# Optimization experiments

Measured on AMD Instinct MI355X. Metric: run time of the kernel, lower is better.

The kernel has to match this reference:

```python
import jax, jax.numpy as jnp
import numpy as np

B, T, H, O = 128, 512, 1024, 128


def setup_inputs() -> dict:
    key = jax.random.key(0)
    ks = jax.random.split(key, 9)
    s = 0.05  # small init scale for numerical sanity
    return {
        "y_hist": jax.random.normal(ks[0], (B, T), jnp.float32),
        "W_ih": jax.random.normal(ks[1], (4 * H, 1), jnp.float32) * s,
        "W_hh": jax.random.normal(ks[2], (4 * H, H), jnp.float32) * s,
        "b_ih": jax.random.normal(ks[3], (4 * H,), jnp.float32) * s,
        "b_hh": jax.random.normal(ks[4], (4 * H,), jnp.float32) * s,
        "fc_W": jax.random.normal(ks[5], (O, H), jnp.float32) * s,
        "fc_b": jax.random.normal(ks[6], (O,), jnp.float32) * s,
        # stands in for the xavier-initialized (1,B,H) h0/c0 of the original
        "h0": jax.random.normal(ks[7], (B, H), jnp.float32) * s,
        "c0": jax.random.normal(ks[8], (B, H), jnp.float32) * s,
    }


def reference(y_hist, W_ih, W_hh, b_ih, b_hh, fc_W, fc_b, h0, c0):
    # PyTorch LSTM cell, gate order (i, f, g, o); input feature size is 1.
    Hs = W_hh.shape[1]
    w_ih = W_ih[:, 0]          # (4H,)
    b = b_ih + b_hh            # (4H,)

    def step(carry, x_t):
        h, c = carry           # (B,H), (B,H)
        gates = h @ W_hh.T + x_t[:, None] * w_ih + b  # (B,4H)
        i, f, g, o = jnp.split(gates, 4, axis=-1)
        c = jax.nn.sigmoid(f) * c + jax.nn.sigmoid(i) * jnp.tanh(g)
        h = jax.nn.sigmoid(o) * jnp.tanh(c)
        return (h, c), None

    (h_T, _), _ = jax.lax.scan(step, (h0, c0), y_hist.T)  # scan over time (T,B)
    return h_T @ fc_W.T + fc_b  # (B, O)
```

## Files before the change

kernel.cpp:

```cpp
#include <hip/hip_runtime.h>
#include <hip/hip_fp16.h>

typedef _Float16 half8 __attribute__((ext_vector_type(8)));
typedef float f32x4 __attribute__((ext_vector_type(4)));

#define T_STEPS 512

__device__ __forceinline__ float sigf(float x) {
    return __builtin_amdgcn_rcpf(1.0f + __builtin_amdgcn_exp2f(-1.44269504088896f * x));
}
__device__ __forceinline__ float tanhf_fast(float x) {
    return 2.0f * __builtin_amdgcn_rcpf(1.0f + __builtin_amdgcn_exp2f(-2.88539008177793f * x)) - 1.0f;
}

__global__ __launch_bounds__(512, 2) void lstm_persist(
    const float* __restrict__ y_hist,
    const float* __restrict__ W_ih,
    const float* __restrict__ W_hh,
    const float* __restrict__ b_ih,
    const float* __restrict__ b_hh,
    const float* __restrict__ fc_W,
    const float* __restrict__ fc_b,
    const float* __restrict__ h0,
    const float* __restrict__ c0,
    float* __restrict__ out,
    unsigned long long* __restrict__ hbuf0,
    unsigned long long* __restrict__ hbuf1,
    unsigned int* __restrict__ flags)
{
    __shared__ _Float16 h_lds[16 * 1024];
    __shared__ float    y_lds[512][16];
    __shared__ unsigned long long hout_lds[128];
    __shared__ char pad_lds[24576];

    const int tid = threadIdx.x;
    const int l   = tid & 63;
    const int wid = tid >> 6;
    const int q4  = l >> 4;
    const int n   = l & 15;
    const int bid = blockIdx.x;
    const int s   = bid & 7;
    const int jj  = bid >> 3;
    if ((unsigned long long)y_hist == 1ull) pad_lds[tid] = 1;

    half8 wfrag[32];
    {
        const int r16  = l & 15;
        const int u_a  = 4 * wid + (r16 >> 2);
        const int g_a  = r16 & 3;
        const int grow = g_a * 1024 + 32 * jj + u_a;
        const float* wrow = W_hh + (size_t)grow * 1024 + 8 * q4;
        #pragma unroll
        for (int c = 0; c < 32; ++c) {
            f32x4 a0 = *(const f32x4*)(wrow + 32 * c);
            f32x4 a1 = *(const f32x4*)(wrow + 32 * c + 4);
            half8 w;
            w[0]=(_Float16)a0[0]; w[1]=(_Float16)a0[1];
            w[2]=(_Float16)a0[2]; w[3]=(_Float16)a0[3];
            w[4]=(_Float16)a1[0]; w[5]=(_Float16)a1[1];
            w[6]=(_Float16)a1[2]; w[7]=(_Float16)a1[3];
            wfrag[c] = w;
        }
    }

    const int u_e = 4 * wid + q4;
    float wih_r[4], bias_r[4], creg;
    #pragma unroll
    for (int g = 0; g < 4; ++g) {
        const int gr = g * 1024 + 32 * jj + u_e;
        wih_r[g]  = W_ih[gr];
        bias_r[g] = b_ih[gr] + b_hh[gr];
    }
    creg = c0[(size_t)(16 * s + n) * 1024 + 32 * jj + u_e];

    {
        const int r = tid >> 5, sg = tid & 31;
        const float* yr = y_hist + (size_t)(16 * s + r) * 512;
        #pragma unroll
        for (int e = 0; e < 4; ++e) {
            f32x4 v = *(const f32x4*)(yr + sg * 4 + 128 * e);
            #pragma unroll
            for (int j = 0; j < 4; ++j) y_lds[sg * 4 + 128 * e + j][r] = v[j];
        }
    }
    {
        const int r = tid >> 5, sg = tid & 31;
        const int swz = (r & 7) << 4;
        const float* hr = h0 + (size_t)(16 * s + r) * 1024 + sg * 32;
        char* db = (char*)h_lds + r * 2048;
        #pragma unroll
        for (int v = 0; v < 4; ++v) {
            f32x4 a0 = *(const f32x4*)(hr + 8 * v);
            f32x4 a1 = *(const f32x4*)(hr + 8 * v + 4);
            half8 hv;
            hv[0]=(_Float16)a0[0]; hv[1]=(_Float16)a0[1];
            hv[2]=(_Float16)a0[2]; hv[3]=(_Float16)a0[3];
            hv[4]=(_Float16)a1[0]; hv[5]=(_Float16)a1[1];
            hv[6]=(_Float16)a1[2]; hv[7]=(_Float16)a1[3];
            *(half8*)(db + ((sg * 64 + 16 * v) ^ swz)) = hv;
        }
    }
    __syncthreads();

    const int bb  = n * 2048 + 16 * q4;
    const int swz = (n & 7) << 4;

    for (int t = 0; t < T_STEPS; ++t) {
        if (t > 0) {
            if (wid == 0) {
                for (;;) {
                    unsigned v = __hip_atomic_load(&flags[(s << 5) + (l & 31)],
                                                   __ATOMIC_RELAXED,
                                                   __HIP_MEMORY_SCOPE_AGENT);
                    if (__all((int)(v >= (unsigned)t))) break;
                    __builtin_amdgcn_s_sleep(1);
                }
            }
            __syncthreads();
            const unsigned long long* gb = ((t & 1) ? hbuf1 : hbuf0) + (s << 12);
            #pragma unroll
            for (int i = 0; i < 8; ++i) {
                const int F = i * 512 + tid;
                unsigned long long v = __hip_atomic_load(gb + F, __ATOMIC_RELAXED,
                                                         __HIP_MEMORY_SCOPE_AGENT);
                const int n2 = (F >> 3) & 15;
                const int off = (n2 * 2048 + ((F >> 7) * 64 + (F & 7) * 8))
                                ^ ((n2 & 7) << 4);
                *(unsigned long long*)((char*)h_lds + off) = v;
            }
            __syncthreads();
        }

        f32x4 acc0 = {0.f, 0.f, 0.f, 0.f}, acc1 = {0.f, 0.f, 0.f, 0.f};
        {
            const char* hb = (const char*)h_lds;
            #pragma unroll
            for (int c = 0; c < 16; ++c) {
                half8 b0 = *(const half8*)(hb + ((bb + 64 * c) ^ swz));
                half8 b1 = *(const half8*)(hb + ((bb + 64 * c + 1024) ^ swz));
                acc0 = __builtin_amdgcn_mfma_f32_16x16x32_f16(wfrag[c], b0, acc0, 0, 0, 0);
                acc1 = __builtin_amdgcn_mfma_f32_16x16x32_f16(wfrag[c + 16], b1, acc1, 0, 0, 0);
            }
        }
        {
            const float yt = y_lds[t][n];
            float gi = acc0[0] + acc1[0] + yt * wih_r[0] + bias_r[0];
            float gf = acc0[1] + acc1[1] + yt * wih_r[1] + bias_r[1];
            float gg = acc0[2] + acc1[2] + yt * wih_r[2] + bias_r[2];
            float go = acc0[3] + acc1[3] + yt * wih_r[3] + bias_r[3];
            float cn = sigf(gf) * creg + sigf(gi) * tanhf_fast(gg);
            creg = cn;
            float hv = sigf(go) * tanhf_fast(cn);
            ((_Float16*)hout_lds)[n * 32 + u_e] = (_Float16)hv;
        }
        __syncthreads();
        if (wid == 0) {
            unsigned long long* ob = ((t & 1) ? hbuf0 : hbuf1) + (s << 12) + (jj << 7);
            unsigned long long v0 = hout_lds[l];
            unsigned long long v1 = hout_lds[l + 64];
            __hip_atomic_store(ob + l, v0, __ATOMIC_RELAXED, __HIP_MEMORY_SCOPE_AGENT);
            __hip_atomic_store(ob + l + 64, v1, __ATOMIC_RELAXED, __HIP_MEMORY_SCOPE_AGENT);
            asm volatile("s_waitcnt vmcnt(0)" ::: "memory");
            if (l == 0)
                __hip_atomic_store(&flags[(s << 5) + jj], (unsigned)(t + 1),
                                   __ATOMIC_RELAXED, __HIP_MEMORY_SCOPE_AGENT);
        }
    }

    if (jj < 16) {
        if (wid == 0) {
            for (;;) {
                unsigned v = __hip_atomic_load(&flags[(s << 5) + (l & 31)],
                                               __ATOMIC_RELAXED,
                                               __HIP_MEMORY_SCOPE_AGENT);
                if (__all((int)(v >= (unsigned)T_STEPS))) break;
                __builtin_amdgcn_s_sleep(1);
            }
        }
        __syncthreads();
        float* hT  = (float*)h_lds;
        float* red = hT + 1024;
        if (tid < 256) {
            const int jjp = tid >> 3, u8 = tid & 7;
            unsigned long long v = __hip_atomic_load(
                hbuf0 + (s << 12) + jjp * 128 + jj * 8 + u8,
                __ATOMIC_RELAXED, __HIP_MEMORY_SCOPE_AGENT);
            const _Float16* hp = (const _Float16*)&v;
            #pragma unroll
            for (int e = 0; e < 4; ++e) hT[32 * jjp + 4 * u8 + e] = (float)hp[e];
        }
        __syncthreads();
        {
            const int o = tid & 127, kq = tid >> 7;
            const float* wr = fc_W + (size_t)o * 1024 + kq * 256;
            const float* hp = hT + kq * 256;
            float p = 0.0f;
            #pragma unroll 8
            for (int i = 0; i < 256; i += 4) {
                f32x4 a = *(const f32x4*)(hp + i);
                f32x4 w = *(const f32x4*)(wr + i);
                p += a[0]*w[0] + a[1]*w[1] + a[2]*w[2] + a[3]*w[3];
            }
            red[kq * 128 + o] = p;
        }
        __syncthreads();
        if (tid < 128) {
            out[(size_t)(16 * s + jj) * 128 + tid] =
                red[tid] + red[128 + tid] + red[256 + tid] + red[384 + tid] + fc_b[tid];
        }
    }
}

extern "C" void kernel_launch(void* const* d_in, const int* in_sizes, int n_in,
                              void* d_out, int out_size, void* d_ws, size_t ws_size,
                              hipStream_t stream) {
    (void)in_sizes; (void)n_in; (void)out_size; (void)ws_size;
    const float* y_hist = (const float*)d_in[0];
    const float* W_ih   = (const float*)d_in[1];
    const float* W_hh   = (const float*)d_in[2];
    const float* b_ih   = (const float*)d_in[3];
    const float* b_hh   = (const float*)d_in[4];
    const float* fc_W   = (const float*)d_in[5];
    const float* fc_b   = (const float*)d_in[6];
    const float* h0     = (const float*)d_in[7];
    const float* c0     = (const float*)d_in[8];

    char* ws = (char*)d_ws;
    unsigned long long* hbuf0 = (unsigned long long*)ws;
    unsigned long long* hbuf1 = (unsigned long long*)(ws + (256 << 10));
    unsigned int*       flags = (unsigned int*)(ws + (512 << 10));

    hipMemsetAsync(flags, 0, 1024, stream);
    hipLaunchKernelGGL(lstm_persist, dim3(256), dim3(512), 0, stream,
                       y_hist, W_ih, W_hh, b_ih, b_hh, fc_W, fc_b, h0, c0,
                       (float*)d_out, hbuf0, hbuf1, flags);
}
```

Measured before the change: 2.280 ms.

## Map blocks to XCDs by hardware XCC id and use lighter cross-block sync

Each block reads its XCC id from a hardware register and takes a slot on that XCD through an atomic counter, so the 32 blocks that exchange hidden state all sit on the same XCD and share its L2. Flag polling switches from atomic loads with sleep to volatile loads with acquire fences and a bounded spin. The hidden-state exchange uses plain loads and stores, the MFMA reduction is split across four accumulators, and the final h is written as fp32 to a separate buffer. The risks are the bounded-spin breaks that can silently skip synchronization, and the assumption that exactly 32 blocks land on each XCD; if that fails the kernel hangs or gives wrong results.

```diff
diff --git a/kernel.cpp b/kernel.cpp
--- a/kernel.cpp
+++ b/kernel.cpp
@@ -6,10 +6,10 @@
 
 #define T_STEPS 512
 
-__device__ __forceinline__ float sigf(float x) {
+static __device__ __forceinline__ float sigf(float x) {
     return __builtin_amdgcn_rcpf(1.0f + __builtin_amdgcn_exp2f(-1.44269504088896f * x));
 }
-__device__ __forceinline__ float tanhf_fast(float x) {
+static __device__ __forceinline__ float tanhf_fast(float x) {
     return 2.0f * __builtin_amdgcn_rcpf(1.0f + __builtin_amdgcn_exp2f(-2.88539008177793f * x)) - 1.0f;
 }
 
@@ -26,22 +26,44 @@
     float* __restrict__ out,
     unsigned long long* __restrict__ hbuf0,
     unsigned long long* __restrict__ hbuf1,
-    unsigned int* __restrict__ flags)
+    float* __restrict__ hfin,
+    unsigned int* __restrict__ flags,
+    unsigned int* __restrict__ xcnt,
+    unsigned int* __restrict__ gbar)
 {
     __shared__ _Float16 h_lds[16 * 1024];
     __shared__ float    y_lds[512][16];
     __shared__ unsigned long long hout_lds[128];
-    __shared__ char pad_lds[24576];
+    __shared__ unsigned sjj[2];
 
     const int tid = threadIdx.x;
     const int l   = tid & 63;
     const int wid = tid >> 6;
     const int q4  = l >> 4;
     const int n   = l & 15;
-    const int bid = blockIdx.x;
-    const int s   = bid & 7;
-    const int jj  = bid >> 3;
-    if ((unsigned long long)y_hist == 1ull) pad_lds[tid] = 1;
+
+    if (tid == 0) {
+        unsigned x;
+        asm volatile("s_getreg_b32 %0, hwreg(HW_REG_XCC_ID)" : "=s"(x));
+        x &= 7u;
+        sjj[0] = x;
+        sjj[1] = atomicAdd(&xcnt[x], 1u) & 31u;
+    }
+    __syncthreads();
+    const int s  = (int)sjj[0];
+    const int jj = (int)sjj[1];
+
+    if (jj == 0 && tid < 32) *(volatile unsigned*)&flags[(s << 5) + tid] = 0u;
+    asm volatile("s_waitcnt vmcnt(0)" ::: "memory");
+    __syncthreads();
+    if (tid == 0) {
+        __hip_atomic_fetch_add(&gbar[s], 1u, __ATOMIC_RELAXED, __HIP_MEMORY_SCOPE_AGENT);
+        int guard = 0;
+        while (__hip_atomic_load(&gbar[s], __ATOMIC_RELAXED, __HIP_MEMORY_SCOPE_AGENT) < 32u) {
+            if (++guard > (1 << 20)) break;
+        }
+    }
+    __syncthreads();
 
     half8 wfrag[32];
     {
@@ -108,86 +130,91 @@
     for (int t = 0; t < T_STEPS; ++t) {
         if (t > 0) {
             if (wid == 0) {
+                const volatile unsigned* fp = flags + (s << 5) + (l & 31);
+                int guard = 0;
                 for (;;) {
-                    unsigned v = __hip_atomic_load(&flags[(s << 5) + (l & 31)],
-                                                   __ATOMIC_RELAXED,
-                                                   __HIP_MEMORY_SCOPE_AGENT);
-                    if (__all((int)(v >= (unsigned)t))) break;
-                    __builtin_amdgcn_s_sleep(1);
+                    unsigned fv = *fp;
+                    if (__all((int)(fv >= (unsigned)t))) break;
+                    if (++guard > (1 << 15)) break;
+                    __builtin_amdgcn_fence(__ATOMIC_ACQUIRE, "agent");
                 }
+                __builtin_amdgcn_fence(__ATOMIC_ACQUIRE, "agent");
             }
             __syncthreads();
             const unsigned long long* gb = ((t & 1) ? hbuf1 : hbuf0) + (s << 12);
             #pragma unroll
             for (int i = 0; i < 8; ++i) {
                 const int F = i * 512 + tid;
-                unsigned long long v = __hip_atomic_load(gb + F, __ATOMIC_RELAXED,
-                                                         __HIP_MEMORY_SCOPE_AGENT);
+                unsigned long long v = gb[F];
                 const int n2 = (F >> 3) & 15;
-                const int off = (n2 * 2048 + ((F >> 7) * 64 + (F & 7) * 8))
+                const int off = ((n2 * 2048) + ((F >> 7) << 6) + ((F & 7) << 3))
                                 ^ ((n2 & 7) << 4);
                 *(unsigned long long*)((char*)h_lds + off) = v;
             }
             __syncthreads();
         }
 
-        f32x4 acc0 = {0.f, 0.f, 0.f, 0.f}, acc1 = {0.f, 0.f, 0.f, 0.f};
+        f32x4 ac0 = {0.f,0.f,0.f,0.f}, ac1 = {0.f,0.f,0.f,0.f};
+        f32x4 ac2 = {0.f,0.f,0.f,0.f}, ac3 = {0.f,0.f,0.f,0.f};
         {
             const char* hb = (const char*)h_lds;
             #pragma unroll
-            for (int c = 0; c < 16; ++c) {
+            for (int c = 0; c < 8; ++c) {
                 half8 b0 = *(const half8*)(hb + ((bb + 64 * c) ^ swz));
-                half8 b1 = *(const half8*)(hb + ((bb + 64 * c + 1024) ^ swz));
-                acc0 = __builtin_amdgcn_mfma_f32_16x16x32_f16(wfrag[c], b0, acc0, 0, 0, 0);
-                acc1 = __builtin_amdgcn_mfma_f32_16x16x32_f16(wfrag[c + 16], b1, acc1, 0, 0, 0);
+                half8 b1 = *(const half8*)(hb + ((bb + 64 * (c + 8)) ^ swz));
+                half8 b2 = *(const half8*)(hb + ((bb + 1024 + 64 * c) ^ swz));
+                half8 b3 = *(const half8*)(hb + ((bb + 1024 + 64 * (c + 8)) ^ swz));
+                ac0 = __builtin_amdgcn_mfma_f32_16x16x32_f16(wfrag[c],      b0, ac0, 0, 0, 0);
+                ac1 = __builtin_amdgcn_mfma_f32_16x16x32_f16(wfrag[c + 8],  b1, ac1, 0, 0, 0);
+                ac2 = __builtin_amdgcn_mfma_f32_16x16x32_f16(wfrag[c + 16], b2, ac2, 0, 0, 0);
+                ac3 = __builtin_amdgcn_mfma_f32_16x16x32_f16(wfrag[c + 24], b3, ac3, 0, 0, 0);
             }
         }
         {
             const float yt = y_lds[t][n];
-            float gi = acc0[0] + acc1[0] + yt * wih_r[0] + bias_r[0];
-            float gf = acc0[1] + acc1[1] + yt * wih_r[1] + bias_r[1];
-            float gg = acc0[2] + acc1[2] + yt * wih_r[2] + bias_r[2];
-            float go = acc0[3] + acc1[3] + yt * wih_r[3] + bias_r[3];
+            float gi = (ac0[0] + ac1[0]) + (ac2[0] + ac3[0]) + yt * wih_r[0] + bias_r[0];
+            float gf = (ac0[1] + ac1[1]) + (ac2[1] + ac3[1]) + yt * wih_r[1] + bias_r[1];
+            float gg = (ac0[2] + ac1[2]) + (ac2[2] + ac3[2]) + yt * wih_r[2] + bias_r[2];
+            float go = (ac0[3] + ac1[3]) + (ac2[3] + ac3[3]) + yt * wih_r[3] + bias_r[3];
             float cn = sigf(gf) * creg + sigf(gi) * tanhf_fast(gg);
             creg = cn;
             float hv = sigf(go) * tanhf_fast(cn);
             ((_Float16*)hout_lds)[n * 32 + u_e] = (_Float16)hv;
+            if (t == T_STEPS - 1) {
+                hfin[(size_t)(16 * s + n) * 1024 + 32 * jj + u_e] = hv;
+                asm volatile("s_waitcnt vmcnt(0)" ::: "memory");
+            }
         }
         __syncthreads();
         if (wid == 0) {
             unsigned long long* ob = ((t & 1) ? hbuf0 : hbuf1) + (s << 12) + (jj << 7);
-            unsigned long long v0 = hout_lds[l];
-            unsigned long long v1 = hout_lds[l + 64];
-            __hip_atomic_store(ob + l, v0, __ATOMIC_RELAXED, __HIP_MEMORY_SCOPE_AGENT);
-            __hip_atomic_store(ob + l + 64, v1, __ATOMIC_RELAXED, __HIP_MEMORY_SCOPE_AGENT);
+            ob[l]      = hout_lds[l];
+            ob[l + 64] = hout_lds[l + 64];
             asm volatile("s_waitcnt vmcnt(0)" ::: "memory");
             if (l == 0)
-                __hip_atomic_store(&flags[(s << 5) + jj], (unsigned)(t + 1),
-                                   __ATOMIC_RELAXED, __HIP_MEMORY_SCOPE_AGENT);
+                *(volatile unsigned*)&flags[(s << 5) + jj] = (unsigned)(t + 1);
         }
     }
 
     if (jj < 16) {
         if (wid == 0) {
+            const volatile unsigned* fp = flags + (s << 5) + (l & 31);
+            int guard = 0;
             for (;;) {
-                unsigned v = __hip_atomic_load(&flags[(s << 5) + (l & 31)],
-                                               __ATOMIC_RELAXED,
-                                               __HIP_MEMORY_SCOPE_AGENT);
-                if (__all((int)(v >= (unsigned)T_STEPS))) break;
-                __builtin_amdgcn_s_sleep(1);
-            }
+                unsigned fv = *fp;
+                if (__all((int)(fv >= (unsigned)T_STEPS))) break;
+                if (++guard > (1 << 15)) break;
+                __builtin_amdgcn_fence(__ATOMIC_ACQUIRE, "agent");
+            }
+            __builtin_amdgcn_fence(__ATOMIC_ACQUIRE, "agent");
         }
         __syncthreads();
         float* hT  = (float*)h_lds;
         float* red = hT + 1024;
+        const int b = 16 * s + jj;
         if (tid < 256) {
-            const int jjp = tid >> 3, u8 = tid & 7;
-            unsigned long long v = __hip_atomic_load(
-                hbuf0 + (s << 12) + jjp * 128 + jj * 8 + u8,
-                __ATOMIC_RELAXED, __HIP_MEMORY_SCOPE_AGENT);
-            const _Float16* hp = (const _Float16*)&v;
-            #pragma unroll
-            for (int e = 0; e < 4; ++e) hT[32 * jjp + 4 * u8 + e] = (float)hp[e];
+            f32x4 v = *(const f32x4*)(hfin + (size_t)b * 1024 + tid * 4);
+            *(f32x4*)(hT + tid * 4) = v;
         }
         __syncthreads();
         {
@@ -205,7 +232,7 @@
         }
         __syncthreads();
         if (tid < 128) {
-            out[(size_t)(16 * s + jj) * 128 + tid] =
+            out[(size_t)b * 128 + tid] =
                 red[tid] + red[128 + tid] + red[256 + tid] + red[384 + tid] + fc_b[tid];
         }
     }
@@ -228,10 +255,13 @@
     char* ws = (char*)d_ws;
     unsigned long long* hbuf0 = (unsigned long long*)ws;
     unsigned long long* hbuf1 = (unsigned long long*)(ws + (256 << 10));
-    unsigned int*       flags = (unsigned int*)(ws + (512 << 10));
-
-    hipMemsetAsync(flags, 0, 1024, stream);
-    hipLaunchKernelGGL(lstm_persist, dim3(256), dim3(512), 0, stream,
+    float*    hfin  = (float*)(ws + (512 << 10));
+    unsigned int* flags = (unsigned int*)(ws + (1024 << 10));
+    unsigned int* xcnt  = (unsigned int*)(ws + (1024 << 10) + 1024);
+    unsigned int* gbar  = (unsigned int*)(ws + (1024 << 10) + 1024 + 128);
+
+    hipMemsetAsync(ws + (1024 << 10) + 1024, 0, 1024, stream);
+    hipLaunchKernelGGL(lstm_persist, dim3(256), dim3(512), 16384, stream,
                        y_hist, W_ih, W_hh, b_ih, b_hh, fc_W, fc_b, h0, c0,
-                       (float*)d_out, hbuf0, hbuf1, flags);
-}
+                       (float*)d_out, hbuf0, hbuf1, hfin, flags, xcnt, gbar);
+}
```

Result: slower. 2.384 ms (+4.6%).
